# Kernel tuning notes

Hardware: AMD Instinct MI355X
Metric: run time of the kernel (lower is better)

The kernel has to match this reference:

```python
import jax, jax.numpy as jnp
import numpy as np

E, H, M, IN, T = 4, 64, 64, 32, 32      # e_size, hidden_state, message, in_size, target
HL = (128, 256, 128)                     # NNet hidden layers (priba's NNet default)
N_LAYERS = 3


def setup_inputs() -> dict:
    key = jax.random.key(0)
    ks = iter(jax.random.split(key, 64))
    B, N = 16, 128

    def w(shape, scale=0.1):
        return jax.random.normal(next(ks), shape, dtype=jnp.float32) * scale

    inp = {
        "h_in": jax.random.normal(next(ks), (B, N, IN), dtype=jnp.float32),
        "am": jax.random.normal(next(ks), (B, N, N, E), dtype=jnp.float32),
        "g_size": jax.random.randint(next(ks), (B,), 0, N),
    }
    # EdgeNetwork NNet: E -> 128 -> 256 -> 128 -> M*H
    dims_e = (E,) + HL + (M * H,)
    for i in range(4):
        inp[f"We{i}"] = w((dims_e[i], dims_e[i + 1]))
        inp[f"be{i}"] = w((dims_e[i + 1],))
    # GRU (torch nn.GRU, one layer, one step): input M, hidden H
    inp["Wih"] = w((3 * H, M)); inp["Whh"] = w((3 * H, H))
    inp["bih"] = w((3 * H,)); inp["bhh"] = w((3 * H,))
    # Readout NNets: i on [h_T, h_0] (H+IN -> T), j on h_T (H -> T)
    dims_i = (H + IN,) + HL + (T,)
    dims_j = (H,) + HL + (T,)
    for i in range(4):
        inp[f"Wi{i}"] = w((dims_i[i], dims_i[i + 1])); inp[f"bi{i}"] = w((dims_i[i + 1],))
        inp[f"Wj{i}"] = w((dims_j[i], dims_j[i + 1])); inp[f"bj{i}"] = w((dims_j[i + 1],))
    return inp


def _mlp(x, Ws, bs):
    for Wk, bk in zip(Ws[:-1], bs[:-1]):
        x = jax.nn.relu(x @ Wk + bk)
    return x @ Ws[-1] + bs[-1]


def reference(h_in, am, g_size,
              We0, be0, We1, be1, We2, be2, We3, be3,
              Wih, Whh, bih, bhh,
              Wi0, bi0, Wi1, bi1, Wi2, bi2, Wi3, bi3,
              Wj0, bj0, Wj1, bj1, Wj2, bj2, Wj3, bj3):
    B, N, _ = h_in.shape
    h = jnp.pad(h_in, ((0, 0), (0, 0), (0, H - IN)))            # pad to hidden size
    mask = (jnp.arange(N)[None, :] < g_size[:, None]).astype(h.dtype)[:, :, None]  # [B,N,1]

    # Edge-network hidden features; final linear layer is fused into the
    # message contraction to avoid materializing per-edge [M,H] matrices.
    f = am                                                       # [B,N,N,E]
    for Wk, bk in ((We0, be0), (We1, be1), (We2, be2)):
        f = jax.nn.relu(f @ Wk + bk)                             # [B,N,N,128]
    W3 = We3.reshape(HL[-1], M, H)                               # [128,M,H]
    b3 = be3.reshape(M, H)

    for _ in range(N_LAYERS):                                    # weight-tied GGNN steps
        # m[b,v,o] = sum_w (A(e_bvw) @ h_bw)[o], A = reshape(f @ We3 + be3)
        t = jnp.einsum('bvwk,bwi->bvki', f, h)                   # [B,N,128,H]
        msg = jnp.einsum('bvki,koi->bvo', t, W3)
        msg = msg + jnp.einsum('oi,bi->bo', b3, h.sum(1))[:, None, :]
        # single-step torch GRU update
        gi = msg @ Wih.T + bih
        gh = h @ Whh.T + bhh
        r = jax.nn.sigmoid(gi[..., :H] + gh[..., :H])
        z = jax.nn.sigmoid(gi[..., H:2 * H] + gh[..., H:2 * H])
        n = jnp.tanh(gi[..., 2 * H:] + r * gh[..., 2 * H:])
        h = (1.0 - z) * n + z * h
        h = h * mask

    # GGNN readout: sum_v mask * sigmoid(i([h_T, h_0])) * j(h_T), then log_softmax
    gate = jax.nn.sigmoid(_mlp(jnp.concatenate([h, h_in], -1),
                               (Wi0, Wi1, Wi2, Wi3), (bi0, bi1, bi2, bi3)))
    val = _mlp(h, (Wj0, Wj1, Wj2, Wj3), (bj0, bj1, bj2, bj3))
    res = (mask * gate * val).sum(1)                             # [B,T]
    return jax.nn.log_softmax(res, axis=1)
```

## Files before the change

kernel.cpp:

```cpp
#include <hip/hip_runtime.h>
#include <math.h>

#define B   16
#define N   128
#define E   4
#define H   64
#define M   64
#define IN_ 32
#define T   32
#define K1  128
#define K2  256
#define K3  128

typedef _Float16 f16;
typedef f16  f16x8 __attribute__((ext_vector_type(8)));
typedef float f32x4 __attribute__((ext_vector_type(4)));

#define MFMA16(a, b, c) __builtin_amdgcn_mfma_f32_16x16x32_f16(a, b, c, 0, 0, 0)

#define OFF_W1T   0
#define OFF_W2T   32768
#define OFF_WE3H  65536
#define OFF_RI0   589824
#define OFF_RI1   602112
#define OFF_RI2   634880
#define OFF_RI3   667648
#define OFF_RJ0   671744
#define OFF_RJ1   679936
#define OFF_RJ2   712704
#define OFF_RJ3   745472
#define WPACK_SZ  749568

union SmemU {
    struct { float xl[64][4]; f16 y1[64][136]; f16 y2[64][264]; } e;
    struct { f16 Al[128][72]; f16 Bl[128][72]; f16 Ol[128][136]; } pg;
    struct { float prt[4][64]; float hsum[64]; float bias[64]; } bi;
};

__global__ __launch_bounds__(256) void prep_kernel(
    const float* __restrict__ h_in,
    const float* __restrict__ We1, const float* __restrict__ We2,
    const float* __restrict__ We3,
    const float* __restrict__ Wi0, const float* __restrict__ Wi1,
    const float* __restrict__ Wi2, const float* __restrict__ Wi3,
    const float* __restrict__ Wj0, const float* __restrict__ Wj1,
    const float* __restrict__ Wj2, const float* __restrict__ Wj3,
    float* __restrict__ h, f16* __restrict__ h16, f16* __restrict__ hin16,
    f16* __restrict__ wp) {
    int idx = blockIdx.x * 256 + threadIdx.x;
    if (idx < B * N * H) {
        int i  = idx & (H - 1);
        int bn = idx >> 6;
        float v = (i < IN_) ? h_in[bn * IN_ + i] : 0.f;
        h[idx] = v;
        h16[idx] = (f16)v;
        if (i < IN_) hin16[bn * IN_ + i] = (f16)v;
    }
    if (idx >= WPACK_SZ) return;
    if (idx < OFF_W2T) {
        int j = idx >> 7, k = idx & 127;
        wp[idx] = (f16)We1[k * 256 + j];
    } else if (idx < OFF_WE3H) {
        int t = idx - OFF_W2T;
        int j = t >> 8, k = t & 255;
        wp[idx] = (f16)We2[k * 128 + j];
    } else if (idx < OFF_RI0) {
        wp[idx] = (f16)We3[idx - OFF_WE3H];
    } else if (idx < OFF_RI1) {
        int t = idx - OFF_RI0;
        int n = t / 96, c = t % 96;
        wp[idx] = (f16)Wi0[c * 128 + n];
    } else if (idx < OFF_RI2) {
        int t = idx - OFF_RI1;
        int n = t >> 7, k = t & 127;
        wp[idx] = (f16)Wi1[k * 256 + n];
    } else if (idx < OFF_RI3) {
        int t = idx - OFF_RI2;
        int n = t >> 8, k = t & 255;
        wp[idx] = (f16)Wi2[k * 128 + n];
    } else if (idx < OFF_RJ0) {
        int t = idx - OFF_RI3;
        int n = t >> 7, k = t & 127;
        wp[idx] = (f16)Wi3[k * 32 + n];
    } else if (idx < OFF_RJ1) {
        int t = idx - OFF_RJ0;
        int n = t >> 6, c = t & 63;
        wp[idx] = (f16)Wj0[c * 128 + n];
    } else if (idx < OFF_RJ2) {
        int t = idx - OFF_RJ1;
        int n = t >> 7, k = t & 127;
        wp[idx] = (f16)Wj1[k * 256 + n];
    } else if (idx < OFF_RJ3) {
        int t = idx - OFF_RJ2;
        int n = t >> 8, k = t & 255;
        wp[idx] = (f16)Wj2[k * 128 + n];
    } else {
        int t = idx - OFF_RJ3;
        int n = t >> 7, k = t & 127;
        wp[idx] = (f16)Wj3[k * 32 + n];
    }
}


__device__ void edge_body(SmemU& su, int tid, int tile,
                          const float* __restrict__ am,
                          const float* __restrict__ We0,
                          const float* __restrict__ be0,
                          const f16* __restrict__ W1t,
                          const float* __restrict__ be1,
                          const f16* __restrict__ W2t,
                          const float* __restrict__ be2,
                          f16* __restrict__ f) {
    int lane = tid & 63, wv = tid >> 6;
    long long g0 = (long long)tile * 64;

    ((float*)su.e.xl)[tid] = am[g0 * 4 + tid];
    __syncthreads();

    {
        int j = tid & 127, e0 = (tid >> 7) * 32;
        float w0 = We0[j], w1 = We0[128 + j], w2 = We0[256 + j], w3 = We0[384 + j];
        float bb = be0[j];
        #pragma unroll 8
        for (int e = e0; e < e0 + 32; ++e) {
            float v = bb + su.e.xl[e][0] * w0 + su.e.xl[e][1] * w1
                         + su.e.xl[e][2] * w2 + su.e.xl[e][3] * w3;
            su.e.y1[e][j] = (f16)fmaxf(v, 0.f);
        }
    }
    __syncthreads();

    int m = lane & 15, q = lane >> 4;

    {
        f32x4 acc[4][4];
        #pragma unroll
        for (int ct = 0; ct < 4; ++ct)
            #pragma unroll
            for (int rt = 0; rt < 4; ++rt) acc[ct][rt] = (f32x4){0.f, 0.f, 0.f, 0.f};
        #pragma unroll
        for (int s = 0; s < 4; ++s) {
            int k0 = s * 32 + q * 8;
            f16x8 afr[4], bfr[4];
            #pragma unroll
            for (int rt = 0; rt < 4; ++rt)
                afr[rt] = *(const f16x8*)&su.e.y1[rt * 16 + m][k0];
            #pragma unroll
            for (int ct = 0; ct < 4; ++ct) {
                int n = (wv * 4 + ct) * 16 + m;
                bfr[ct] = *(const f16x8*)(W1t + n * 128 + k0);
            }
            #pragma unroll
            for (int ct = 0; ct < 4; ++ct)
                #pragma unroll
                for (int rt = 0; rt < 4; ++rt)
                    acc[ct][rt] = MFMA16(afr[rt], bfr[ct], acc[ct][rt]);
        }
        #pragma unroll
        for (int ct = 0; ct < 4; ++ct) {
            int n = (wv * 4 + ct) * 16 + m;
            float bb = be1[n];
            #pragma unroll
            for (int rt = 0; rt < 4; ++rt)
                #pragma unroll
                for (int r = 0; r < 4; ++r) {
                    int row = rt * 16 + q * 4 + r;
                    su.e.y2[row][n] = (f16)fmaxf(acc[ct][rt][r] + bb, 0.f);
                }
        }
    }
    __syncthreads();

    {
        f32x4 acc[2][4];
        #pragma unroll
        for (int ct = 0; ct < 2; ++ct)
            #pragma unroll
            for (int rt = 0; rt < 4; ++rt) acc[ct][rt] = (f32x4){0.f, 0.f, 0.f, 0.f};
        #pragma unroll
        for (int s = 0; s < 8; ++s) {
            int k0 = s * 32 + q * 8;
            f16x8 afr[4], bfr[2];
            #pragma unroll
            for (int rt = 0; rt < 4; ++rt)
                afr[rt] = *(const f16x8*)&su.e.y2[rt * 16 + m][k0];
            #pragma unroll
            for (int ct = 0; ct < 2; ++ct) {
                int n = (wv * 2 + ct) * 16 + m;
                bfr[ct] = *(const f16x8*)(W2t + n * 256 + k0);
            }
            #pragma unroll
            for (int ct = 0; ct < 2; ++ct)
                #pragma unroll
                for (int rt = 0; rt < 4; ++rt)
                    acc[ct][rt] = MFMA16(afr[rt], bfr[ct], acc[ct][rt]);
        }
        #pragma unroll
        for (int ct = 0; ct < 2; ++ct) {
            int n = (wv * 2 + ct) * 16 + m;
            float bb = be2[n];
            #pragma unroll
            for (int rt = 0; rt < 4; ++rt)
                #pragma unroll
                for (int r = 0; r < 4; ++r) {
                    int row = rt * 16 + q * 4 + r;
                    su.e.y1[row][n] = (f16)fmaxf(acc[ct][rt][r] + bb, 0.f);
                }
        }
    }
    __syncthreads();

    #pragma unroll
    for (int j = 0; j < 4; ++j) {
        int c = tid + j * 256;
        int e = c >> 4, pp = c & 15;
        *(uint4*)(f + (g0 + e) * 128 + pp * 8) = *(const uint4*)&su.e.y1[e][pp * 8];
    }
}

__device__ void pgemm_body(SmemU& su, int tid, int ob, int nt,
                           const f16* __restrict__ h16,
                           const f16* __restrict__ We3h,
                           f16* __restrict__ P2) {
    int lane = tid & 63, wv = tid >> 6;

    #pragma unroll
    for (int j = 0; j < 4; ++j) {
        int c = tid + j * 256;
        int row = c >> 3, pp = c & 7;
        *(uint4*)&su.pg.Al[row][pp * 8] =
            *(const uint4*)(h16 + (size_t)(nt * 128 + row) * 64 + pp * 8);
    }
    #pragma unroll
    for (int j = 0; j < 4; ++j) {
        int c = tid + j * 256;
        int k = c >> 3, pp = c & 7;
        *(uint4*)&su.pg.Bl[k][pp * 8] =
            *(const uint4*)(We3h + ((size_t)(k * 64 + ob)) * 64 + pp * 8);
    }
    __syncthreads();

    int m = lane & 15, q = lane >> 4;
    f32x4 acc[2][8];
    #pragma unroll
    for (int ct = 0; ct < 2; ++ct)
        #pragma unroll
        for (int rt = 0; rt < 8; ++rt) acc[ct][rt] = (f32x4){0.f, 0.f, 0.f, 0.f};
    #pragma unroll
    for (int s = 0; s < 2; ++s) {
        int k0 = s * 32 + q * 8;
        f16x8 afr[8], bfr[2];
        #pragma unroll
        for (int rt = 0; rt < 8; ++rt)
            afr[rt] = *(const f16x8*)&su.pg.Al[rt * 16 + m][k0];
        #pragma unroll
        for (int ct = 0; ct < 2; ++ct)
            bfr[ct] = *(const f16x8*)&su.pg.Bl[(wv * 2 + ct) * 16 + m][k0];
        #pragma unroll
        for (int ct = 0; ct < 2; ++ct)
            #pragma unroll
            for (int rt = 0; rt < 8; ++rt)
                acc[ct][rt] = MFMA16(afr[rt], bfr[ct], acc[ct][rt]);
    }
    #pragma unroll
    for (int ct = 0; ct < 2; ++ct) {
        int col = (wv * 2 + ct) * 16 + m;
        #pragma unroll
        for (int rt = 0; rt < 8; ++rt)
            #pragma unroll
            for (int r = 0; r < 4; ++r)
                su.pg.Ol[rt * 16 + q * 4 + r][col] = (f16)acc[ct][rt][r];
    }
    __syncthreads();
    #pragma unroll
    for (int j = 0; j < 8; ++j) {
        int c = tid + j * 256;
        int row = c >> 4, pp = c & 15;
        *(uint4*)(P2 + ((size_t)(nt * 128 + row) * 64 + ob) * 128 + pp * 8) =
            *(const uint4*)&su.pg.Ol[row][pp * 8];
    }
}

__device__ void bias_body(SmemU& su, int tid, int b,
                          const float* __restrict__ h,
                          const float* __restrict__ be3,
                          float* __restrict__ biasb) {
    int i = tid & 63, wq = tid >> 6;
    float s = 0.f;
    for (int w = wq; w < N; w += 4) s += h[((size_t)(b * N + w)) * H + i];
    su.bi.prt[wq][i] = s;
    __syncthreads();
    if (tid < 64)
        su.bi.hsum[tid] = su.bi.prt[0][tid] + su.bi.prt[1][tid]
                        + su.bi.prt[2][tid] + su.bi.prt[3][tid];
    __syncthreads();
    if (tid < 64) {
        float sb = 0.f;
        #pragma unroll 4
        for (int ii = 0; ii < H; ++ii) sb += be3[tid * H + ii] * su.bi.hsum[ii];
        biasb[b * 64 + tid] = sb;
    }
}

__global__ __launch_bounds__(256, 2) void mega0_kernel(
    const float* __restrict__ am,
    const float* __restrict__ We0, const float* __restrict__ be0,
    const float* __restrict__ be1, const float* __restrict__ be2,
    const float* __restrict__ be3,
    const f16* __restrict__ wp,
    const float* __restrict__ h, const f16* __restrict__ h16,
    f16* __restrict__ f, f16* __restrict__ P2, float* __restrict__ biasb) {
    __shared__ SmemU su;
    int tid = threadIdx.x;
    int bid = blockIdx.x;
    if (bid < 4096) {
        edge_body(su, tid, bid, am, We0, be0, wp + OFF_W1T, be1, wp + OFF_W2T,
                  be2, f);
    } else if (bid < 5120) {
        int t = bid - 4096;
        pgemm_body(su, tid, t & 63, t >> 6, h16, wp + OFF_WE3H, P2);
    } else {
        bias_body(su, tid, bid - 5120, h, be3, biasb);
    }
}

__global__ __launch_bounds__(256, 2) void pg_bias_kernel(
    const float* __restrict__ be3, const f16* __restrict__ wp,
    const float* __restrict__ h, const f16* __restrict__ h16,
    f16* __restrict__ P2, float* __restrict__ biasb) {
    __shared__ SmemU su;
    int tid = threadIdx.x;
    int bid = blockIdx.x;
    if (bid < 1024) {
        pgemm_body(su, tid, bid & 63, bid >> 6, h16, wp + OFF_WE3H, P2);
    } else {
        bias_body(su, tid, bid - 1024, h, be3, biasb);
    }
}

__global__ __launch_bounds__(256, 2) void msg_mfma(
    const f16* __restrict__ f, const f16* __restrict__ P2,
    float* __restrict__ part) {
    __shared__ f16 Al[128][136];
    __shared__ f16 Bl[64][136];
    int tid = threadIdx.x, lane = tid & 63, wv = tid >> 6;
    int ws = blockIdx.x;
    int b  = blockIdx.y;
    int m = lane & 15, q = lane >> 4;

    f32x4 acc[2][4];
    #pragma unroll
    for (int rt = 0; rt < 2; ++rt)
        #pragma unroll
        for (int ct = 0; ct < 4; ++ct) acc[rt][ct] = (f32x4){0.f, 0.f, 0.f, 0.f};

    for (int wi = 0; wi < 4; ++wi) {
        int w = ws * 4 + wi;
        #pragma unroll
        for (int j = 0; j < 8; ++j) {
            int c = tid + j * 256;
            int v = c >> 4, pp = c & 15;
            *(uint4*)&Al[v][pp * 8] =
                *(const uint4*)(f + (((size_t)(b * 128 + v) * 128 + w) * 128) + pp * 8);
        }
        #pragma unroll
        for (int j = 0; j < 4; ++j) {
            int c = tid + j * 256;
            int o = c >> 4, pp = c & 15;
            *(uint4*)&Bl[o][pp * 8] =
                *(const uint4*)(P2 + (((size_t)(b * 128 + w) * 64 + o) * 128) + pp * 8);
        }
        __syncthreads();
        #pragma unroll
        for (int s = 0; s < 4; ++s) {
            int k0 = s * 32 + q * 8;
            f16x8 afr[2], bfr[4];
            #pragma unroll
            for (int rt = 0; rt < 2; ++rt)
                afr[rt] = *(const f16x8*)&Al[(wv * 2 + rt) * 16 + m][k0];
            #pragma unroll
            for (int ct = 0; ct < 4; ++ct)
                bfr[ct] = *(const f16x8*)&Bl[ct * 16 + m][k0];
            #pragma unroll
            for (int rt = 0; rt < 2; ++rt)
                #pragma unroll
                for (int ct = 0; ct < 4; ++ct)
                    acc[rt][ct] = MFMA16(afr[rt], bfr[ct], acc[rt][ct]);
        }
        __syncthreads();
    }
    float* pp = part + (size_t)ws * (2048 * 64);
    #pragma unroll
    for (int rt = 0; rt < 2; ++rt)
        #pragma unroll
        for (int ct = 0; ct < 4; ++ct) {
            int o = ct * 16 + m;
            #pragma unroll
            for (int r = 0; r < 4; ++r) {
                int v = (wv * 2 + rt) * 16 + q * 4 + r;
                pp[(size_t)(b * 128 + v) * 64 + o] = acc[rt][ct][r];
            }
        }
}

__global__ __launch_bounds__(192) void gru_kernel(
    const float* __restrict__ biasb, const float* __restrict__ part,
    float* __restrict__ h, f16* __restrict__ h16,
    const float* __restrict__ Wih, const float* __restrict__ Whh,
    const float* __restrict__ bih, const float* __restrict__ bhh,
    const int* __restrict__ g_size) {
    __shared__ float m_lds[M];
    __shared__ float h_lds[H];
    __shared__ float gi[3 * H], gh[3 * H];
    int tid = threadIdx.x;
    int bv  = blockIdx.x;
    int b = bv >> 7, v = bv & 127;

    if (tid < M) {
        float s = biasb[b * 64 + tid];
        #pragma unroll 8
        for (int sp = 0; sp < 32; ++sp)
            s += part[(size_t)sp * (2048 * 64) + bv * 64 + tid];
        m_lds[tid] = s;
    } else if (tid < M + H) {
        h_lds[tid - M] = h[bv * H + (tid - M)];
    }
    __syncthreads();

    {
        float si = bih[tid], sh = bhh[tid];
        const float* wi = Wih + tid * M;
        const float* wh = Whh + tid * H;
        #pragma unroll 4
        for (int k = 0; k < M; ++k) si += wi[k] * m_lds[k];
        #pragma unroll 4
        for (int k = 0; k < H; ++k) sh += wh[k] * h_lds[k];
        gi[tid] = si;
        gh[tid] = sh;
    }
    __syncthreads();
    if (tid < H) {
        float r = 1.f / (1.f + expf(-(gi[tid] + gh[tid])));
        float z = 1.f / (1.f + expf(-(gi[H + tid] + gh[H + tid])));
        float n = tanhf(gi[2 * H + tid] + r * gh[2 * H + tid]);
        float hv = (1.f - z) * n + z * h_lds[tid];
        float maskf = (v < g_size[b]) ? 1.f : 0.f;
        hv *= maskf;
        h[bv * H + tid] = hv;
        h16[bv * H + tid] = (f16)hv;
    }
}

__global__ __launch_bounds__(256, 4) void readout_mfma(
    const f16* __restrict__ h16, const f16* __restrict__ hin16,
    const int* __restrict__ g_size, const f16* __restrict__ wp,
    const float* __restrict__ bi0, const float* __restrict__ bi1,
    const float* __restrict__ bi2, const float* __restrict__ bi3,
    const float* __restrict__ bj0, const float* __restrict__ bj1,
    const float* __restrict__ bj2, const float* __restrict__ bj3,
    float* __restrict__ contrib) {
    __shared__ f16 Xl[32][104];
    __shared__ f16 A1[32][136];
    __shared__ f16 A2[32][264];
    __shared__ float Gl[32][36];
    const f16* Ri0 = wp + OFF_RI0; const f16* Ri1 = wp + OFF_RI1;
    const f16* Ri2 = wp + OFF_RI2; const f16* Ri3 = wp + OFF_RI3;
    const f16* Rj0 = wp + OFF_RJ0; const f16* Rj1 = wp + OFF_RJ1;
    const f16* Rj2 = wp + OFF_RJ2; const f16* Rj3 = wp + OFF_RJ3;
    int tid = threadIdx.x, lane = tid & 63, wv = tid >> 6;
    int m = lane & 15, q = lane >> 4;
    int r0 = blockIdx.x * 32;

    {
        int row = tid >> 3, pp = tid & 7;
        *(uint4*)&Xl[row][pp * 8] = *(const uint4*)(h16 + (size_t)(r0 + row) * 64 + pp * 8);
        if (tid < 128) {
            int row2 = tid >> 2, p2 = tid & 3;
            *(uint4*)&Xl[row2][64 + p2 * 8] =
                *(const uint4*)(hin16 + (size_t)(r0 + row2) * 32 + p2 * 8);
        }
    }
    __syncthreads();

    {
        f32x4 acc[2][2];
        #pragma unroll
        for (int ct = 0; ct < 2; ++ct)
            #pragma unroll
            for (int rt = 0; rt < 2; ++rt) acc[ct][rt] = (f32x4){0.f, 0.f, 0.f, 0.f};
        #pragma unroll
        for (int s = 0; s < 3; ++s) {
            int k0 = s * 32 + q * 8;
            f16x8 afr[2], bfr[2];
            #pragma unroll
            for (int rt = 0; rt < 2; ++rt) afr[rt] = *(const f16x8*)&Xl[rt * 16 + m][k0];
            #pragma unroll
            for (int ct = 0; ct < 2; ++ct)
                bfr[ct] = *(const f16x8*)(Ri0 + ((wv * 2 + ct) * 16 + m) * 96 + k0);
            #pragma unroll
            for (int ct = 0; ct < 2; ++ct)
                #pragma unroll
                for (int rt = 0; rt < 2; ++rt)
                    acc[ct][rt] = MFMA16(afr[rt], bfr[ct], acc[ct][rt]);
        }
        #pragma unroll
        for (int ct = 0; ct < 2; ++ct) {
            int n = (wv * 2 + ct) * 16 + m;
            float bb = bi0[n];
            #pragma unroll
            for (int rt = 0; rt < 2; ++rt)
                #pragma unroll
                for (int r = 0; r < 4; ++r)
                    A1[rt * 16 + q * 4 + r][n] = (f16)fmaxf(acc[ct][rt][r] + bb, 0.f);
        }
    }
    __syncthreads();

    {
        f32x4 acc[4][2];
        #pragma unroll
        for (int ct = 0; ct < 4; ++ct)
            #pragma unroll
            for (int rt = 0; rt < 2; ++rt) acc[ct][rt] = (f32x4){0.f, 0.f, 0.f, 0.f};
        #pragma unroll
        for (int s = 0; s < 4; ++s) {
            int k0 = s * 32 + q * 8;
            f16x8 afr[2], bfr[4];
            #pragma unroll
            for (int rt = 0; rt < 2; ++rt) afr[rt] = *(const f16x8*)&A1[rt * 16 + m][k0];
            #pragma unroll
            for (int ct = 0; ct < 4; ++ct)
                bfr[ct] = *(const f16x8*)(Ri1 + ((wv * 4 + ct) * 16 + m) * 128 + k0);
            #pragma unroll
            for (int ct = 0; ct < 4; ++ct)
                #pragma unroll
                for (int rt = 0; rt < 2; ++rt)
                    acc[ct][rt] = MFMA16(afr[rt], bfr[ct], acc[ct][rt]);
        }
        #pragma unroll
        for (int ct = 0; ct < 4; ++ct) {
            int n = (wv * 4 + ct) * 16 + m;
            float bb = bi1[n];
            #pragma unroll
            for (int rt = 0; rt < 2; ++rt)
                #pragma unroll
                for (int r = 0; r < 4; ++r)
                    A2[rt * 16 + q * 4 + r][n] = (f16)fmaxf(acc[ct][rt][r] + bb, 0.f);
        }
    }
    __syncthreads();

    {
        f32x4 acc[2][2];
        #pragma unroll
        for (int ct = 0; ct < 2; ++ct)
            #pragma unroll
            for (int rt = 0; rt < 2; ++rt) acc[ct][rt] = (f32x4){0.f, 0.f, 0.f, 0.f};
        #pragma unroll
        for (int s = 0; s < 8; ++s) {
            int k0 = s * 32 + q * 8;
            f16x8 afr[2], bfr[2];
            #pragma unroll
            for (int rt = 0; rt < 2; ++rt) afr[rt] = *(const f16x8*)&A2[rt * 16 + m][k0];
            #pragma unroll
            for (int ct = 0; ct < 2; ++ct)
                bfr[ct] = *(const f16x8*)(Ri2 + ((wv * 2 + ct) * 16 + m) * 256 + k0);
            #pragma unroll
            for (int ct = 0; ct < 2; ++ct)
                #pragma unroll
                for (int rt = 0; rt < 2; ++rt)
                    acc[ct][rt] = MFMA16(afr[rt], bfr[ct], acc[ct][rt]);
        }
        __syncthreads();
        #pragma unroll
        for (int ct = 0; ct < 2; ++ct) {
            int n = (wv * 2 + ct) * 16 + m;
            float bb = bi2[n];
            #pragma unroll
            for (int rt = 0; rt < 2; ++rt)
                #pragma unroll
                for (int r = 0; r < 4; ++r)
                    A1[rt * 16 + q * 4 + r][n] = (f16)fmaxf(acc[ct][rt][r] + bb, 0.f);
        }
    }
    __syncthreads();

    if (wv < 2) {
        f32x4 acc[2];
        acc[0] = (f32x4){0.f, 0.f, 0.f, 0.f};
        acc[1] = (f32x4){0.f, 0.f, 0.f, 0.f};
        int n = wv * 16 + m;
        #pragma unroll
        for (int s = 0; s < 4; ++s) {
            int k0 = s * 32 + q * 8;
            f16x8 bfr = *(const f16x8*)(Ri3 + n * 128 + k0);
            #pragma unroll
            for (int rt = 0; rt < 2; ++rt) {
                f16x8 afr = *(const f16x8*)&A1[rt * 16 + m][k0];
                acc[rt] = MFMA16(afr, bfr, acc[rt]);
            }
        }
        float bb = bi3[n];
        #pragma unroll
        for (int rt = 0; rt < 2; ++rt)
            #pragma unroll
            for (int r = 0; r < 4; ++r)
                Gl[rt * 16 + q * 4 + r][n] = 1.f / (1.f + expf(-(acc[rt][r] + bb)));
    }
    __syncthreads();

    {
        f32x4 acc[2][2];
        #pragma unroll
        for (int ct = 0; ct < 2; ++ct)
            #pragma unroll
            for (int rt = 0; rt < 2; ++rt) acc[ct][rt] = (f32x4){0.f, 0.f, 0.f, 0.f};
        #pragma unroll
        for (int s = 0; s < 2; ++s) {
            int k0 = s * 32 + q * 8;
            f16x8 afr[2], bfr[2];
            #pragma unroll
            for (int rt = 0; rt < 2; ++rt) afr[rt] = *(const f16x8*)&Xl[rt * 16 + m][k0];
            #pragma unroll
            for (int ct = 0; ct < 2; ++ct)
                bfr[ct] = *(const f16x8*)(Rj0 + ((wv * 2 + ct) * 16 + m) * 64 + k0);
            #pragma unroll
            for (int ct = 0; ct < 2; ++ct)
                #pragma unroll
                for (int rt = 0; rt < 2; ++rt)
                    acc[ct][rt] = MFMA16(afr[rt], bfr[ct], acc[ct][rt]);
        }
        __syncthreads();
        #pragma unroll
        for (int ct = 0; ct < 2; ++ct) {
            int n = (wv * 2 + ct) * 16 + m;
            float bb = bj0[n];
            #pragma unroll
            for (int rt = 0; rt < 2; ++rt)
                #pragma unroll
                for (int r = 0; r < 4; ++r)
                    A1[rt * 16 + q * 4 + r][n] = (f16)fmaxf(acc[ct][rt][r] + bb, 0.f);
        }
    }
    __syncthreads();

    {
        f32x4 acc[4][2];
        #pragma unroll
        for (int ct = 0; ct < 4; ++ct)
            #pragma unroll
            for (int rt = 0; rt < 2; ++rt) acc[ct][rt] = (f32x4){0.f, 0.f, 0.f, 0.f};
        #pragma unroll
        for (int s = 0; s < 4; ++s) {
            int k0 = s * 32 + q * 8;
            f16x8 afr[2], bfr[4];
            #pragma unroll
            for (int rt = 0; rt < 2; ++rt) afr[rt] = *(const f16x8*)&A1[rt * 16 + m][k0];
            #pragma unroll
            for (int ct = 0; ct < 4; ++ct)
                bfr[ct] = *(const f16x8*)(Rj1 + ((wv * 4 + ct) * 16 + m) * 128 + k0);
            #pragma unroll
            for (int ct = 0; ct < 4; ++ct)
                #pragma unroll
                for (int rt = 0; rt < 2; ++rt)
                    acc[ct][rt] = MFMA16(afr[rt], bfr[ct], acc[ct][rt]);
        }
        #pragma unroll
        for (int ct = 0; ct < 4; ++ct) {
            int n = (wv * 4 + ct) * 16 + m;
            float bb = bj1[n];
            #pragma unroll
            for (int rt = 0; rt < 2; ++rt)
                #pragma unroll
                for (int r = 0; r < 4; ++r)
                    A2[rt * 16 + q * 4 + r][n] = (f16)fmaxf(acc[ct][rt][r] + bb, 0.f);
        }
    }
    __syncthreads();

    {
        f32x4 acc[2][2];
        #pragma unroll
        for (int ct = 0; ct < 2; ++ct)
            #pragma unroll
            for (int rt = 0; rt < 2; ++rt) acc[ct][rt] = (f32x4){0.f, 0.f, 0.f, 0.f};
        #pragma unroll
        for (int s = 0; s < 8; ++s) {
            int k0 = s * 32 + q * 8;
            f16x8 afr[2], bfr[2];
            #pragma unroll
            for (int rt = 0; rt < 2; ++rt) afr[rt] = *(const f16x8*)&A2[rt * 16 + m][k0];
            #pragma unroll
            for (int ct = 0; ct < 2; ++ct)
                bfr[ct] = *(const f16x8*)(Rj2 + ((wv * 2 + ct) * 16 + m) * 256 + k0);
            #pragma unroll
            for (int ct = 0; ct < 2; ++ct)
                #pragma unroll
                for (int rt = 0; rt < 2; ++rt)
                    acc[ct][rt] = MFMA16(afr[rt], bfr[ct], acc[ct][rt]);
        }
        __syncthreads();
        #pragma unroll
        for (int ct = 0; ct < 2; ++ct) {
            int n = (wv * 2 + ct) * 16 + m;
            float bb = bj2[n];
            #pragma unroll
            for (int rt = 0; rt < 2; ++rt)
                #pragma unroll
                for (int r = 0; r < 4; ++r)
                    A1[rt * 16 + q * 4 + r][n] = (f16)fmaxf(acc[ct][rt][r] + bb, 0.f);
        }
    }
    __syncthreads();

    if (wv < 2) {
        f32x4 acc[2];
        acc[0] = (f32x4){0.f, 0.f, 0.f, 0.f};
        acc[1] = (f32x4){0.f, 0.f, 0.f, 0.f};
        int n = wv * 16 + m;
        #pragma unroll
        for (int s = 0; s < 4; ++s) {
            int k0 = s * 32 + q * 8;
            f16x8 bfr = *(const f16x8*)(Rj3 + n * 128 + k0);
            #pragma unroll
            for (int rt = 0; rt < 2; ++rt) {
                f16x8 afr = *(const f16x8*)&A1[rt * 16 + m][k0];
                acc[rt] = MFMA16(afr, bfr, acc[rt]);
            }
        }
        float bb = bj3[n];
        #pragma unroll
        for (int rt = 0; rt < 2; ++rt)
            #pragma unroll
            for (int r = 0; r < 4; ++r) {
                int row = rt * 16 + q * 4 + r;
                int rg = r0 + row;
                int b = rg >> 7, v = rg & 127;
                float maskf = (v < g_size[b]) ? 1.f : 0.f;
                contrib[(size_t)rg * T + n] = maskf * Gl[row][n] * (acc[rt][r] + bb);
            }
    }
}

__global__ __launch_bounds__(64) void finalize_kernel(const float* __restrict__ contrib,
                                                      float* __restrict__ out) {
    __shared__ float res[T];
    int b = blockIdx.x;
    int o = threadIdx.x;
    if (o < T) {
        float s = 0.f;
        for (int v = 0; v < N; ++v) s += contrib[(b * N + v) * T + o];
        res[o] = s;
    }
    __syncthreads();
    if (o < T) {
        float mx = res[0];
        for (int i = 1; i < T; ++i) mx = fmaxf(mx, res[i]);
        float se = 0.f;
        for (int i = 0; i < T; ++i) se += expf(res[i] - mx);
        out[b * T + o] = res[o] - mx - logf(se);
    }
}

extern "C" void kernel_launch(void* const* d_in, const int* in_sizes, int n_in,
                              void* d_out, int out_size, void* d_ws, size_t ws_size,
                              hipStream_t stream) {
    (void)in_sizes; (void)n_in; (void)out_size; (void)ws_size;
    const float* h_in = (const float*)d_in[0];
    const float* am   = (const float*)d_in[1];
    const int*   g_sz = (const int*)d_in[2];
    const float* We0 = (const float*)d_in[3],  *be0 = (const float*)d_in[4];
    const float* We1 = (const float*)d_in[5],  *be1 = (const float*)d_in[6];
    const float* We2 = (const float*)d_in[7],  *be2 = (const float*)d_in[8];
    const float* We3 = (const float*)d_in[9],  *be3 = (const float*)d_in[10];
    const float* Wih = (const float*)d_in[11], *Whh = (const float*)d_in[12];
    const float* bih = (const float*)d_in[13], *bhh = (const float*)d_in[14];
    const float* Wi0 = (const float*)d_in[15], *bi0 = (const float*)d_in[16];
    const float* Wj0 = (const float*)d_in[17], *bj0 = (const float*)d_in[18];
    const float* Wi1 = (const float*)d_in[19], *bi1 = (const float*)d_in[20];
    const float* Wj1 = (const float*)d_in[21], *bj1 = (const float*)d_in[22];
    const float* Wi2 = (const float*)d_in[23], *bi2 = (const float*)d_in[24];
    const float* Wj2 = (const float*)d_in[25], *bj2 = (const float*)d_in[26];
    const float* Wi3 = (const float*)d_in[27], *bi3 = (const float*)d_in[28];
    const float* Wj3 = (const float*)d_in[29], *bj3 = (const float*)d_in[30];

    float* out = (float*)d_out;

    f16*   f    = (f16*)d_ws;
    f16*   P2   = f + (size_t)33554432;
    float* part = (float*)(P2 + (size_t)16777216);
    float* h    = part + (size_t)4194304;
    float* biasb = h + 131072;
    float* contrib = biasb + 1024;
    f16*   h16  = (f16*)(contrib + 65536);
    f16*   hin16 = h16 + 131072;
    f16*   wp   = hin16 + 65536;

    prep_kernel<<<(WPACK_SZ + 255) / 256, 256, 0, stream>>>(
        h_in, We1, We2, We3, Wi0, Wi1, Wi2, Wi3, Wj0, Wj1, Wj2, Wj3,
        h, h16, hin16, wp);

    mega0_kernel<<<4096 + 1024 + 16, 256, 0, stream>>>(
        am, We0, be0, be1, be2, be3, wp, h, h16, f, P2, biasb);
    msg_mfma<<<dim3(32, 16), 256, 0, stream>>>(f, P2, part);
    gru_kernel<<<B * N, 192, 0, stream>>>(biasb, part, h, h16,
                                          Wih, Whh, bih, bhh, g_sz);

    for (int l = 1; l < 3; ++l) {
        pg_bias_kernel<<<1024 + 16, 256, 0, stream>>>(be3, wp, h, h16, P2, biasb);
        msg_mfma<<<dim3(32, 16), 256, 0, stream>>>(f, P2, part);
        gru_kernel<<<B * N, 192, 0, stream>>>(biasb, part, h, h16,
                                              Wih, Whh, bih, bhh, g_sz);
    }

    readout_mfma<<<64, 256, 0, stream>>>(h16, hin16, g_sz, wp,
                                         bi0, bi1, bi2, bi3,
                                         bj0, bj1, bj2, bj3, contrib);
    finalize_kernel<<<B, 64, 0, stream>>>(contrib, out);
}
```

Before: 412.1 us.

## Fuse all stages into one persistent kernel with software grid barriers

```diff
diff --git a/kernel.cpp b/kernel.cpp
--- a/kernel.cpp
+++ b/kernel.cpp
@@ -8,9 +8,6 @@
 #define M   64
 #define IN_ 32
 #define T   32
-#define K1  128
-#define K2  256
-#define K3  128
 
 typedef _Float16 f16;
 typedef f16  f16x8 __attribute__((ext_vector_type(8)));
@@ -31,96 +28,56 @@
 #define OFF_RJ3   745472
 #define WPACK_SZ  749568
 
+#define GRID_BLKS 256
+
 union SmemU {
     struct { float xl[64][4]; f16 y1[64][136]; f16 y2[64][264]; } e;
     struct { f16 Al[128][72]; f16 Bl[128][72]; f16 Ol[128][136]; } pg;
     struct { float prt[4][64]; float hsum[64]; float bias[64]; } bi;
+    struct { f16 Al[128][136]; f16 Bl[64][136]; } mm;
+    struct { f16 Xl[32][104]; f16 A1[32][136]; f16 A2[32][264]; float Gl[32][36]; } ro;
+    struct { float m_lds[64]; float h_lds[64]; float gi[192]; float gh[192]; } gr;
+    float fin[32];
 };
 
-__global__ __launch_bounds__(256) void prep_kernel(
-    const float* __restrict__ h_in,
-    const float* __restrict__ We1, const float* __restrict__ We2,
-    const float* __restrict__ We3,
-    const float* __restrict__ Wi0, const float* __restrict__ Wi1,
-    const float* __restrict__ Wi2, const float* __restrict__ Wi3,
-    const float* __restrict__ Wj0, const float* __restrict__ Wj1,
-    const float* __restrict__ Wj2, const float* __restrict__ Wj3,
-    float* __restrict__ h, f16* __restrict__ h16, f16* __restrict__ hin16,
-    f16* __restrict__ wp) {
-    int idx = blockIdx.x * 256 + threadIdx.x;
-    if (idx < B * N * H) {
-        int i  = idx & (H - 1);
-        int bn = idx >> 6;
-        float v = (i < IN_) ? h_in[bn * IN_ + i] : 0.f;
-        h[idx] = v;
-        h16[idx] = (f16)v;
-        if (i < IN_) hin16[bn * IN_ + i] = (f16)v;
-    }
-    if (idx >= WPACK_SZ) return;
-    if (idx < OFF_W2T) {
-        int j = idx >> 7, k = idx & 127;
-        wp[idx] = (f16)We1[k * 256 + j];
-    } else if (idx < OFF_WE3H) {
-        int t = idx - OFF_W2T;
-        int j = t >> 8, k = t & 255;
-        wp[idx] = (f16)We2[k * 128 + j];
-    } else if (idx < OFF_RI0) {
-        wp[idx] = (f16)We3[idx - OFF_WE3H];
-    } else if (idx < OFF_RI1) {
-        int t = idx - OFF_RI0;
-        int n = t / 96, c = t % 96;
-        wp[idx] = (f16)Wi0[c * 128 + n];
-    } else if (idx < OFF_RI2) {
-        int t = idx - OFF_RI1;
-        int n = t >> 7, k = t & 127;
-        wp[idx] = (f16)Wi1[k * 256 + n];
-    } else if (idx < OFF_RI3) {
-        int t = idx - OFF_RI2;
-        int n = t >> 8, k = t & 255;
-        wp[idx] = (f16)Wi2[k * 128 + n];
-    } else if (idx < OFF_RJ0) {
-        int t = idx - OFF_RI3;
-        int n = t >> 7, k = t & 127;
-        wp[idx] = (f16)Wi3[k * 32 + n];
-    } else if (idx < OFF_RJ1) {
-        int t = idx - OFF_RJ0;
-        int n = t >> 6, c = t & 63;
-        wp[idx] = (f16)Wj0[c * 128 + n];
-    } else if (idx < OFF_RJ2) {
-        int t = idx - OFF_RJ1;
-        int n = t >> 7, k = t & 127;
-        wp[idx] = (f16)Wj1[k * 256 + n];
-    } else if (idx < OFF_RJ3) {
-        int t = idx - OFF_RJ2;
-        int n = t >> 8, k = t & 255;
-        wp[idx] = (f16)Wj2[k * 128 + n];
-    } else {
-        int t = idx - OFF_RJ3;
-        int n = t >> 7, k = t & 127;
-        wp[idx] = (f16)Wj3[k * 32 + n];
-    }
-}
-
-
-__device__ void edge_body(SmemU& su, int tid, int tile,
-                          const float* __restrict__ am,
-                          const float* __restrict__ We0,
-                          const float* __restrict__ be0,
-                          const f16* __restrict__ W1t,
-                          const float* __restrict__ be1,
-                          const f16* __restrict__ W2t,
-                          const float* __restrict__ be2,
-                          f16* __restrict__ f) {
+struct Params {
+    const float *h_in, *am;
+    const int   *g_sz;
+    const float *We0, *be0, *We1, *be1, *We2, *be2, *We3, *be3;
+    const float *Wih, *Whh, *bih, *bhh;
+    const float *bi0, *bi1, *bi2, *bi3, *bj0, *bj1, *bj2, *bj3;
+    const float *Wi0, *Wi1, *Wi2, *Wi3, *Wj0, *Wj1, *Wj2, *Wj3;
+    f16   *f, *P2, *h16, *hin16, *wp;
+    float *msg, *h, *contrib, *out;
+    int   *bar;
+};
+
+__device__ __forceinline__ void gbar(int* bar, int ph, int tid) {
+    __syncthreads();
+    __threadfence();
+    if (tid == 0) {
+        atomicAdd(&bar[ph], 1);
+        while (atomicAdd(&bar[ph], 0) < GRID_BLKS)
+            __builtin_amdgcn_s_sleep(2);
+    }
+    __syncthreads();
+    __threadfence();
+}
+
+
+__device__ void edge_task(SmemU& su, int tid, int tile, const Params& p) {
     int lane = tid & 63, wv = tid >> 6;
     long long g0 = (long long)tile * 64;
-
-    ((float*)su.e.xl)[tid] = am[g0 * 4 + tid];
+    const f16* W1t = p.wp + OFF_W1T;
+    const f16* W2t = p.wp + OFF_W2T;
+
+    ((float*)su.e.xl)[tid] = p.am[g0 * 4 + tid];
     __syncthreads();
 
     {
         int j = tid & 127, e0 = (tid >> 7) * 32;
-        float w0 = We0[j], w1 = We0[128 + j], w2 = We0[256 + j], w3 = We0[384 + j];
-        float bb = be0[j];
+        float w0 = p.We0[j], w1 = p.We0[128 + j], w2 = p.We0[256 + j], w3 = p.We0[384 + j];
+        float bb = p.be0[j];
         #pragma unroll 8
         for (int e = e0; e < e0 + 32; ++e) {
             float v = bb + su.e.xl[e][0] * w0 + su.e.xl[e][1] * w1
@@ -159,7 +116,7 @@
         #pragma unroll
         for (int ct = 0; ct < 4; ++ct) {
             int n = (wv * 4 + ct) * 16 + m;
-            float bb = be1[n];
+            float bb = p.be1[n];
             #pragma unroll
             for (int rt = 0; rt < 4; ++rt)
                 #pragma unroll
@@ -198,7 +155,7 @@
         #pragma unroll
         for (int ct = 0; ct < 2; ++ct) {
             int n = (wv * 2 + ct) * 16 + m;
-            float bb = be2[n];
+            float bb = p.be2[n];
             #pragma unroll
             for (int rt = 0; rt < 4; ++rt)
                 #pragma unroll
@@ -214,22 +171,20 @@
     for (int j = 0; j < 4; ++j) {
         int c = tid + j * 256;
         int e = c >> 4, pp = c & 15;
-        *(uint4*)(f + (g0 + e) * 128 + pp * 8) = *(const uint4*)&su.e.y1[e][pp * 8];
-    }
-}
-
-__device__ void pgemm_body(SmemU& su, int tid, int ob, int nt,
-                           const f16* __restrict__ h16,
-                           const f16* __restrict__ We3h,
-                           f16* __restrict__ P2) {
+        *(uint4*)(p.f + (g0 + e) * 128 + pp * 8) = *(const uint4*)&su.e.y1[e][pp * 8];
+    }
+}
+
+__device__ void pgemm_task(SmemU& su, int tid, int ob, int nt, const Params& p) {
     int lane = tid & 63, wv = tid >> 6;
+    const f16* We3h = p.wp + OFF_WE3H;
 
     #pragma unroll
     for (int j = 0; j < 4; ++j) {
         int c = tid + j * 256;
         int row = c >> 3, pp = c & 7;
         *(uint4*)&su.pg.Al[row][pp * 8] =
-            *(const uint4*)(h16 + (size_t)(nt * 128 + row) * 64 + pp * 8);
+            *(const uint4*)(p.h16 + (size_t)(nt * 128 + row) * 64 + pp * 8);
     }
     #pragma unroll
     for (int j = 0; j < 4; ++j) {
@@ -276,18 +231,15 @@
     for (int j = 0; j < 8; ++j) {
         int c = tid + j * 256;
         int row = c >> 4, pp = c & 15;
-        *(uint4*)(P2 + ((size_t)(nt * 128 + row) * 64 + ob) * 128 + pp * 8) =
+        *(uint4*)(p.P2 + ((size_t)(nt * 128 + row) * 64 + ob) * 128 + pp * 8) =
             *(const uint4*)&su.pg.Ol[row][pp * 8];
     }
 }
 
-__device__ void bias_body(SmemU& su, int tid, int b,
-                          const float* __restrict__ h,
-                          const float* __restrict__ be3,
-                          float* __restrict__ biasb) {
+__device__ void bias_task(SmemU& su, int tid, int b, const Params& p) {
     int i = tid & 63, wq = tid >> 6;
     float s = 0.f;
-    for (int w = wq; w < N; w += 4) s += h[((size_t)(b * N + w)) * H + i];
+    for (int w = wq; w < N; w += 4) s += p.h[((size_t)(b * N + w)) * H + i];
     su.bi.prt[wq][i] = s;
     __syncthreads();
     if (tid < 64)
@@ -297,55 +249,16 @@
     if (tid < 64) {
         float sb = 0.f;
         #pragma unroll 4
-        for (int ii = 0; ii < H; ++ii) sb += be3[tid * H + ii] * su.bi.hsum[ii];
-        biasb[b * 64 + tid] = sb;
-    }
-}
-
-__global__ __launch_bounds__(256, 2) void mega0_kernel(
-    const float* __restrict__ am,
-    const float* __restrict__ We0, const float* __restrict__ be0,
-    const float* __restrict__ be1, const float* __restrict__ be2,
-    const float* __restrict__ be3,
-    const f16* __restrict__ wp,
-    const float* __restrict__ h, const f16* __restrict__ h16,
-    f16* __restrict__ f, f16* __restrict__ P2, float* __restrict__ biasb) {
-    __shared__ SmemU su;
-    int tid = threadIdx.x;
-    int bid = blockIdx.x;
-    if (bid < 4096) {
-        edge_body(su, tid, bid, am, We0, be0, wp + OFF_W1T, be1, wp + OFF_W2T,
-                  be2, f);
-    } else if (bid < 5120) {
-        int t = bid - 4096;
-        pgemm_body(su, tid, t & 63, t >> 6, h16, wp + OFF_WE3H, P2);
-    } else {
-        bias_body(su, tid, bid - 5120, h, be3, biasb);
-    }
-}
-
-__global__ __launch_bounds__(256, 2) void pg_bias_kernel(
-    const float* __restrict__ be3, const f16* __restrict__ wp,
-    const float* __restrict__ h, const f16* __restrict__ h16,
-    f16* __restrict__ P2, float* __restrict__ biasb) {
-    __shared__ SmemU su;
-    int tid = threadIdx.x;
-    int bid = blockIdx.x;
-    if (bid < 1024) {
-        pgemm_body(su, tid, bid & 63, bid >> 6, h16, wp + OFF_WE3H, P2);
-    } else {
-        bias_body(su, tid, bid - 1024, h, be3, biasb);
-    }
-}
-
-__global__ __launch_bounds__(256, 2) void msg_mfma(
-    const f16* __restrict__ f, const f16* __restrict__ P2,
-    float* __restrict__ part) {
-    __shared__ f16 Al[128][136];
-    __shared__ f16 Bl[64][136];
-    int tid = threadIdx.x, lane = tid & 63, wv = tid >> 6;
-    int ws = blockIdx.x;
-    int b  = blockIdx.y;
+        for (int ii = 0; ii < H; ++ii) sb += p.be3[tid * H + ii] * su.bi.hsum[ii];
+        su.bi.bias[tid] = sb;
+    }
+    __syncthreads();
+    for (int idx = tid; idx < N * M; idx += 256)
+        p.msg[(size_t)b * N * M + idx] = su.bi.bias[idx & 63];
+}
+
+__device__ void msg_task(SmemU& su, int tid, int ws, int b, const Params& p) {
+    int lane = tid & 63, wv = tid >> 6;
     int m = lane & 15, q = lane >> 4;
 
     f32x4 acc[2][4];
@@ -360,15 +273,15 @@
         for (int j = 0; j < 8; ++j) {
             int c = tid + j * 256;
             int v = c >> 4, pp = c & 15;
-            *(uint4*)&Al[v][pp * 8] =
-                *(const uint4*)(f + (((size_t)(b * 128 + v) * 128 + w) * 128) + pp * 8);
+            *(uint4*)&su.mm.Al[v][pp * 8] =
+                *(const uint4*)(p.f + (((size_t)(b * 128 + v) * 128 + w) * 128) + pp * 8);
         }
         #pragma unroll
         for (int j = 0; j < 4; ++j) {
             int c = tid + j * 256;
             int o = c >> 4, pp = c & 15;
-            *(uint4*)&Bl[o][pp * 8] =
-                *(const uint4*)(P2 + (((size_t)(b * 128 + w) * 64 + o) * 128) + pp * 8);
+            *(uint4*)&su.mm.Bl[o][pp * 8] =
+                *(const uint4*)(p.P2 + (((size_t)(b * 128 + w) * 64 + o) * 128) + pp * 8);
         }
         __syncthreads();
         #pragma unroll
@@ -377,10 +290,10 @@
             f16x8 afr[2], bfr[4];
             #pragma unroll
             for (int rt = 0; rt < 2; ++rt)
-                afr[rt] = *(const f16x8*)&Al[(wv * 2 + rt) * 16 + m][k0];
+                afr[rt] = *(const f16x8*)&su.mm.Al[(wv * 2 + rt) * 16 + m][k0];
             #pragma unroll
             for (int ct = 0; ct < 4; ++ct)
-                bfr[ct] = *(const f16x8*)&Bl[ct * 16 + m][k0];
+                bfr[ct] = *(const f16x8*)&su.mm.Bl[ct * 16 + m][k0];
             #pragma unroll
             for (int rt = 0; rt < 2; ++rt)
                 #pragma unroll
@@ -389,7 +302,6 @@
         }
         __syncthreads();
     }
-    float* pp = part + (size_t)ws * (2048 * 64);
     #pragma unroll
     for (int rt = 0; rt < 2; ++rt)
         #pragma unroll
@@ -398,86 +310,58 @@
             #pragma unroll
             for (int r = 0; r < 4; ++r) {
                 int v = (wv * 2 + rt) * 16 + q * 4 + r;
-                pp[(size_t)(b * 128 + v) * 64 + o] = acc[rt][ct][r];
+                atomicAdd(p.msg + (size_t)(b * 128 + v) * 64 + o, acc[rt][ct][r]);
             }
         }
 }
 
-__global__ __launch_bounds__(192) void gru_kernel(
-    const float* __restrict__ biasb, const float* __restrict__ part,
-    float* __restrict__ h, f16* __restrict__ h16,
-    const float* __restrict__ Wih, const float* __restrict__ Whh,
-    const float* __restrict__ bih, const float* __restrict__ bhh,
-    const int* __restrict__ g_size) {
-    __shared__ float m_lds[M];
-    __shared__ float h_lds[H];
-    __shared__ float gi[3 * H], gh[3 * H];
-    int tid = threadIdx.x;
-    int bv  = blockIdx.x;
+__device__ void gru_node(SmemU& su, int tid, int bv, const Params& p) {
     int b = bv >> 7, v = bv & 127;
-
-    if (tid < M) {
-        float s = biasb[b * 64 + tid];
-        #pragma unroll 8
-        for (int sp = 0; sp < 32; ++sp)
-            s += part[(size_t)sp * (2048 * 64) + bv * 64 + tid];
-        m_lds[tid] = s;
-    } else if (tid < M + H) {
-        h_lds[tid - M] = h[bv * H + (tid - M)];
-    }
-    __syncthreads();
-
-    {
-        float si = bih[tid], sh = bhh[tid];
-        const float* wi = Wih + tid * M;
-        const float* wh = Whh + tid * H;
+    if (tid < 64) su.gr.m_lds[tid] = p.msg[(size_t)bv * 64 + tid];
+    else if (tid < 128) su.gr.h_lds[tid - 64] = p.h[bv * 64 + (tid - 64)];
+    __syncthreads();
+    if (tid < 192) {
+        float si = p.bih[tid], sh = p.bhh[tid];
+        const float* wi = p.Wih + tid * M;
+        const float* wh = p.Whh + tid * H;
         #pragma unroll 4
-        for (int k = 0; k < M; ++k) si += wi[k] * m_lds[k];
+        for (int k = 0; k < M; ++k) si += wi[k] * su.gr.m_lds[k];
         #pragma unroll 4
-        for (int k = 0; k < H; ++k) sh += wh[k] * h_lds[k];
-        gi[tid] = si;
-        gh[tid] = sh;
-    }
-    __syncthreads();
-    if (tid < H) {
-        float r = 1.f / (1.f + expf(-(gi[tid] + gh[tid])));
-        float z = 1.f / (1.f + expf(-(gi[H + tid] + gh[H + tid])));
-        float n = tanhf(gi[2 * H + tid] + r * gh[2 * H + tid]);
-        float hv = (1.f - z) * n + z * h_lds[tid];
-        float maskf = (v < g_size[b]) ? 1.f : 0.f;
+        for (int k = 0; k < H; ++k) sh += wh[k] * su.gr.h_lds[k];
+        su.gr.gi[tid] = si;
+        su.gr.gh[tid] = sh;
+    }
+    __syncthreads();
+    if (tid < 64) {
+        float r = 1.f / (1.f + expf(-(su.gr.gi[tid] + su.gr.gh[tid])));
+        float z = 1.f / (1.f + expf(-(su.gr.gi[64 + tid] + su.gr.gh[64 + tid])));
+        float n = tanhf(su.gr.gi[128 + tid] + r * su.gr.gh[128 + tid]);
+        float hv = (1.f - z) * n + z * su.gr.h_lds[tid];
+        float maskf = (v < p.g_sz[b]) ? 1.f : 0.f;
         hv *= maskf;
-        h[bv * H + tid] = hv;
-        h16[bv * H + tid] = (f16)hv;
-    }
-}
-
-__global__ __launch_bounds__(256, 4) void readout_mfma(
-    const f16* __restrict__ h16, const f16* __restrict__ hin16,
-    const int* __restrict__ g_size, const f16* __restrict__ wp,
-    const float* __restrict__ bi0, const float* __restrict__ bi1,
-    const float* __restrict__ bi2, const float* __restrict__ bi3,
-    const float* __restrict__ bj0, const float* __restrict__ bj1,
-    const float* __restrict__ bj2, const float* __restrict__ bj3,
-    float* __restrict__ contrib) {
-    __shared__ f16 Xl[32][104];
-    __shared__ f16 A1[32][136];
-    __shared__ f16 A2[32][264];
-    __shared__ float Gl[32][36];
-    const f16* Ri0 = wp + OFF_RI0; const f16* Ri1 = wp + OFF_RI1;
-    const f16* Ri2 = wp + OFF_RI2; const f16* Ri3 = wp + OFF_RI3;
-    const f16* Rj0 = wp + OFF_RJ0; const f16* Rj1 = wp + OFF_RJ1;
-    const f16* Rj2 = wp + OFF_RJ2; const f16* Rj3 = wp + OFF_RJ3;
-    int tid = threadIdx.x, lane = tid & 63, wv = tid >> 6;
+        p.h[bv * 64 + tid] = hv;
+        p.h16[bv * 64 + tid] = (f16)hv;
+    }
+    __syncthreads();
+}
+
+__device__ void readout_task(SmemU& su, int tid, int blk, const Params& p) {
+    const f16* Ri0 = p.wp + OFF_RI0; const f16* Ri1 = p.wp + OFF_RI1;
+    const f16* Ri2 = p.wp + OFF_RI2; const f16* Ri3 = p.wp + OFF_RI3;
+    const f16* Rj0 = p.wp + OFF_RJ0; const f16* Rj1 = p.wp + OFF_RJ1;
+    const f16* Rj2 = p.wp + OFF_RJ2; const f16* Rj3 = p.wp + OFF_RJ3;
+    int lane = tid & 63, wv = tid >> 6;
     int m = lane & 15, q = lane >> 4;
-    int r0 = blockIdx.x * 32;
+    int r0 = blk * 32;
 
     {
         int row = tid >> 3, pp = tid & 7;
-        *(uint4*)&Xl[row][pp * 8] = *(const uint4*)(h16 + (size_t)(r0 + row) * 64 + pp * 8);
+        *(uint4*)&su.ro.Xl[row][pp * 8] =
+            *(const uint4*)(p.h16 + (size_t)(r0 + row) * 64 + pp * 8);
         if (tid < 128) {
             int row2 = tid >> 2, p2 = tid & 3;
-            *(uint4*)&Xl[row2][64 + p2 * 8] =
-                *(const uint4*)(hin16 + (size_t)(r0 + row2) * 32 + p2 * 8);
+            *(uint4*)&su.ro.Xl[row2][64 + p2 * 8] =
+                *(const uint4*)(p.hin16 + (size_t)(r0 + row2) * 32 + p2 * 8);
         }
     }
     __syncthreads();
@@ -493,7 +377,8 @@
             int k0 = s * 32 + q * 8;
             f16x8 afr[2], bfr[2];
             #pragma unroll
-            for (int rt = 0; rt < 2; ++rt) afr[rt] = *(const f16x8*)&Xl[rt * 16 + m][k0];
+            for (int rt = 0; rt < 2; ++rt)
+                afr[rt] = *(const f16x8*)&su.ro.Xl[rt * 16 + m][k0];
             #pragma unroll
             for (int ct = 0; ct < 2; ++ct)
                 bfr[ct] = *(const f16x8*)(Ri0 + ((wv * 2 + ct) * 16 + m) * 96 + k0);
@@ -506,12 +391,12 @@
         #pragma unroll
         for (int ct = 0; ct < 2; ++ct) {
             int n = (wv * 2 + ct) * 16 + m;
-            float bb = bi0[n];
+            float bb = p.bi0[n];
             #pragma unroll
             for (int rt = 0; rt < 2; ++rt)
                 #pragma unroll
                 for (int r = 0; r < 4; ++r)
-                    A1[rt * 16 + q * 4 + r][n] = (f16)fmaxf(acc[ct][rt][r] + bb, 0.f);
+                    su.ro.A1[rt * 16 + q * 4 + r][n] = (f16)fmaxf(acc[ct][rt][r] + bb, 0.f);
         }
     }
     __syncthreads();
@@ -527,7 +412,8 @@
             int k0 = s * 32 + q * 8;
             f16x8 afr[2], bfr[4];
             #pragma unroll
-            for (int rt = 0; rt < 2; ++rt) afr[rt] = *(const f16x8*)&A1[rt * 16 + m][k0];
+            for (int rt = 0; rt < 2; ++rt)
+                afr[rt] = *(const f16x8*)&su.ro.A1[rt * 16 + m][k0];
             #pragma unroll
             for (int ct = 0; ct < 4; ++ct)
                 bfr[ct] = *(const f16x8*)(Ri1 + ((wv * 4 + ct) * 16 + m) * 128 + k0);
@@ -540,12 +426,12 @@
         #pragma unroll
         for (int ct = 0; ct < 4; ++ct) {
             int n = (wv * 4 + ct) * 16 + m;
-            float bb = bi1[n];
+            float bb = p.bi1[n];
             #pragma unroll
             for (int rt = 0; rt < 2; ++rt)
                 #pragma unroll
                 for (int r = 0; r < 4; ++r)
-                    A2[rt * 16 + q * 4 + r][n] = (f16)fmaxf(acc[ct][rt][r] + bb, 0.f);
+                    su.ro.A2[rt * 16 + q * 4 + r][n] = (f16)fmaxf(acc[ct][rt][r] + bb, 0.f);
         }
     }
     __syncthreads();
@@ -561,7 +447,8 @@
             int k0 = s * 32 + q * 8;
             f16x8 afr[2], bfr[2];
             #pragma unroll
-            for (int rt = 0; rt < 2; ++rt) afr[rt] = *(const f16x8*)&A2[rt * 16 + m][k0];
+            for (int rt = 0; rt < 2; ++rt)
+                afr[rt] = *(const f16x8*)&su.ro.A2[rt * 16 + m][k0];
             #pragma unroll
             for (int ct = 0; ct < 2; ++ct)
                 bfr[ct] = *(const f16x8*)(Ri2 + ((wv * 2 + ct) * 16 + m) * 256 + k0);
@@ -575,12 +462,12 @@
         #pragma unroll
         for (int ct = 0; ct < 2; ++ct) {
             int n = (wv * 2 + ct) * 16 + m;
-            float bb = bi2[n];
+            float bb = p.bi2[n];
             #pragma unroll
             for (int rt = 0; rt < 2; ++rt)
                 #pragma unroll
                 for (int r = 0; r < 4; ++r)
-                    A1[rt * 16 + q * 4 + r][n] = (f16)fmaxf(acc[ct][rt][r] + bb, 0.f);
+                    su.ro.A1[rt * 16 + q * 4 + r][n] = (f16)fmaxf(acc[ct][rt][r] + bb, 0.f);
         }
     }
     __syncthreads();
@@ -596,16 +483,16 @@
             f16x8 bfr = *(const f16x8*)(Ri3 + n * 128 + k0);
             #pragma unroll
             for (int rt = 0; rt < 2; ++rt) {
-                f16x8 afr = *(const f16x8*)&A1[rt * 16 + m][k0];
+                f16x8 afr = *(const f16x8*)&su.ro.A1[rt * 16 + m][k0];
                 acc[rt] = MFMA16(afr, bfr, acc[rt]);
             }
         }
-        float bb = bi3[n];
+        float bb = p.bi3[n];
         #pragma unroll
         for (int rt = 0; rt < 2; ++rt)
             #pragma unroll
             for (int r = 0; r < 4; ++r)
-                Gl[rt * 16 + q * 4 + r][n] = 1.f / (1.f + expf(-(acc[rt][r] + bb)));
+                su.ro.Gl[rt * 16 + q * 4 + r][n] = 1.f / (1.f + expf(-(acc[rt][r] + bb)));
     }
     __syncthreads();
 
@@ -620,7 +507,8 @@
             int k0 = s * 32 + q * 8;
             f16x8 afr[2], bfr[2];
             #pragma unroll
-            for (int rt = 0; rt < 2; ++rt) afr[rt] = *(const f16x8*)&Xl[rt * 16 + m][k0];
+            for (int rt = 0; rt < 2; ++rt)
+                afr[rt] = *(const f16x8*)&su.ro.Xl[rt * 16 + m][k0];
             #pragma unroll
             for (int ct = 0; ct < 2; ++ct)
                 bfr[ct] = *(const f16x8*)(Rj0 + ((wv * 2 + ct) * 16 + m) * 64 + k0);
@@ -634,12 +522,12 @@
         #pragma unroll
         for (int ct = 0; ct < 2; ++ct) {
             int n = (wv * 2 + ct) * 16 + m;
-            float bb = bj0[n];
+            float bb = p.bj0[n];
             #pragma unroll
             for (int rt = 0; rt < 2; ++rt)
                 #pragma unroll
                 for (int r = 0; r < 4; ++r)
-                    A1[rt * 16 + q * 4 + r][n] = (f16)fmaxf(acc[ct][rt][r] + bb, 0.f);
+                    su.ro.A1[rt * 16 + q * 4 + r][n] = (f16)fmaxf(acc[ct][rt][r] + bb, 0.f);
         }
     }
     __syncthreads();
@@ -655,7 +543,8 @@
             int k0 = s * 32 + q * 8;
             f16x8 afr[2], bfr[4];
             #pragma unroll
-            for (int rt = 0; rt < 2; ++rt) afr[rt] = *(const f16x8*)&A1[rt * 16 + m][k0];
+            for (int rt = 0; rt < 2; ++rt)
+                afr[rt] = *(const f16x8*)&su.ro.A1[rt * 16 + m][k0];
             #pragma unroll
             for (int ct = 0; ct < 4; ++ct)
                 bfr[ct] = *(const f16x8*)(Rj1 + ((wv * 4 + ct) * 16 + m) * 128 + k0);
@@ -668,12 +557,12 @@
         #pragma unroll
         for (int ct = 0; ct < 4; ++ct) {
             int n = (wv * 4 + ct) * 16 + m;
-            float bb = bj1[n];
+            float bb = p.bj1[n];
             #pragma unroll
             for (int rt = 0; rt < 2; ++rt)
                 #pragma unroll
                 for (int r = 0; r < 4; ++r)
-                    A2[rt * 16 + q * 4 + r][n] = (f16)fmaxf(acc[ct][rt][r] + bb, 0.f);
+                    su.ro.A2[rt * 16 + q * 4 + r][n] = (f16)fmaxf(acc[ct][rt][r] + bb, 0.f);
         }
     }
     __syncthreads();
@@ -689,7 +578,8 @@
             int k0 = s * 32 + q * 8;
             f16x8 afr[2], bfr[2];
             #pragma unroll
-            for (int rt = 0; rt < 2; ++rt) afr[rt] = *(const f16x8*)&A2[rt * 16 + m][k0];
+            for (int rt = 0; rt < 2; ++rt)
+                afr[rt] = *(const f16x8*)&su.ro.A2[rt * 16 + m][k0];
             #pragma unroll
             for (int ct = 0; ct < 2; ++ct)
                 bfr[ct] = *(const f16x8*)(Rj2 + ((wv * 2 + ct) * 16 + m) * 256 + k0);
@@ -703,12 +593,12 @@
         #pragma unroll
         for (int ct = 0; ct < 2; ++ct) {
             int n = (wv * 2 + ct) * 16 + m;
-            float bb = bj2[n];
+            float bb = p.bj2[n];
             #pragma unroll
             for (int rt = 0; rt < 2; ++rt)
                 #pragma unroll
                 for (int r = 0; r < 4; ++r)
-                    A1[rt * 16 + q * 4 + r][n] = (f16)fmaxf(acc[ct][rt][r] + bb, 0.f);
+                    su.ro.A1[rt * 16 + q * 4 + r][n] = (f16)fmaxf(acc[ct][rt][r] + bb, 0.f);
         }
     }
     __syncthreads();
@@ -724,11 +614,11 @@
             f16x8 bfr = *(const f16x8*)(Rj3 + n * 128 + k0);
             #pragma unroll
             for (int rt = 0; rt < 2; ++rt) {
-                f16x8 afr = *(const f16x8*)&A1[rt * 16 + m][k0];
+                f16x8 afr = *(const f16x8*)&su.ro.A1[rt * 16 + m][k0];
                 acc[rt] = MFMA16(afr, bfr, acc[rt]);
             }
         }
-        float bb = bj3[n];
+        float bb = p.bj3[n];
         #pragma unroll
         for (int rt = 0; rt < 2; ++rt)
             #pragma unroll
@@ -736,85 +626,162 @@
                 int row = rt * 16 + q * 4 + r;
                 int rg = r0 + row;
                 int b = rg >> 7, v = rg & 127;
-                float maskf = (v < g_size[b]) ? 1.f : 0.f;
-                contrib[(size_t)rg * T + n] = maskf * Gl[row][n] * (acc[rt][r] + bb);
+                float maskf = (v < p.g_sz[b]) ? 1.f : 0.f;
+                p.contrib[(size_t)rg * T + n] = maskf * su.ro.Gl[row][n] * (acc[rt][r] + bb);
             }
     }
-}
-
-__global__ __launch_bounds__(64) void finalize_kernel(const float* __restrict__ contrib,
-                                                      float* __restrict__ out) {
-    __shared__ float res[T];
-    int b = blockIdx.x;
-    int o = threadIdx.x;
-    if (o < T) {
+    __syncthreads();
+}
+
+__device__ void finalize_task(SmemU& su, int tid, int b, const Params& p) {
+    if (tid < T) {
         float s = 0.f;
-        for (int v = 0; v < N; ++v) s += contrib[(b * N + v) * T + o];
-        res[o] = s;
-    }
-    __syncthreads();
-    if (o < T) {
-        float mx = res[0];
-        for (int i = 1; i < T; ++i) mx = fmaxf(mx, res[i]);
+        for (int v = 0; v < N; ++v) s += p.contrib[(b * N + v) * T + tid];
+        su.fin[tid] = s;
+    }
+    __syncthreads();
+    if (tid < T) {
+        float mx = su.fin[0];
+        for (int i = 1; i < T; ++i) mx = fmaxf(mx, su.fin[i]);
         float se = 0.f;
-        for (int i = 0; i < T; ++i) se += expf(res[i] - mx);
-        out[b * T + o] = res[o] - mx - logf(se);
-    }
+        for (int i = 0; i < T; ++i) se += expf(su.fin[i] - mx);
+        p.out[b * T + tid] = su.fin[tid] - mx - logf(se);
+    }
+    __syncthreads();
+}
+
+__global__ __launch_bounds__(256) void mega_kernel(Params p) {
+    __shared__ SmemU su;
+    int tid = threadIdx.x;
+    int bid = blockIdx.x;
+    int gidx = bid * 256 + tid;
+
+    for (int idx = gidx; idx < B * N * H; idx += GRID_BLKS * 256) {
+        int i  = idx & (H - 1);
+        int bn = idx >> 6;
+        float v = (i < IN_) ? p.h_in[bn * IN_ + i] : 0.f;
+        p.h[idx] = v;
+        p.h16[idx] = (f16)v;
+        if (i < IN_) p.hin16[bn * IN_ + i] = (f16)v;
+    }
+    for (int idx = gidx; idx < WPACK_SZ; idx += GRID_BLKS * 256) {
+        f16* wp = p.wp;
+        if (idx < OFF_W2T) {
+            int j = idx >> 7, k = idx & 127;
+            wp[idx] = (f16)p.We1[k * 256 + j];
+        } else if (idx < OFF_WE3H) {
+            int t = idx - OFF_W2T;
+            int j = t >> 8, k = t & 255;
+            wp[idx] = (f16)p.We2[k * 128 + j];
+        } else if (idx < OFF_RI0) {
+            wp[idx] = (f16)p.We3[idx - OFF_WE3H];
+        } else if (idx < OFF_RI1) {
+            int t = idx - OFF_RI0;
+            int n = t / 96, c = t % 96;
+            wp[idx] = (f16)p.Wi0[c * 128 + n];
+        } else if (idx < OFF_RI2) {
+            int t = idx - OFF_RI1;
+            int n = t >> 7, k = t & 127;
+            wp[idx] = (f16)p.Wi1[k * 256 + n];
+        } else if (idx < OFF_RI3) {
+            int t = idx - OFF_RI2;
+            int n = t >> 8, k = t & 255;
+            wp[idx] = (f16)p.Wi2[k * 128 + n];
+        } else if (idx < OFF_RJ0) {
+            int t = idx - OFF_RI3;
+            int n = t >> 7, k = t & 127;
+            wp[idx] = (f16)p.Wi3[k * 32 + n];
+        } else if (idx < OFF_RJ1) {
+            int t = idx - OFF_RJ0;
+            int n = t >> 6, c = t & 63;
+            wp[idx] = (f16)p.Wj0[c * 128 + n];
+        } else if (idx < OFF_RJ2) {
+            int t = idx - OFF_RJ1;
+            int n = t >> 7, k = t & 127;
+            wp[idx] = (f16)p.Wj1[k * 256 + n];
+        } else if (idx < OFF_RJ3) {
+            int t = idx - OFF_RJ2;
+            int n = t >> 8, k = t & 255;
+            wp[idx] = (f16)p.Wj2[k * 128 + n];
+        } else {
+            int t = idx - OFF_RJ3;
+            int n = t >> 7, k = t & 127;
+            wp[idx] = (f16)p.Wj3[k * 32 + n];
+        }
+    }
+    int ph = 0;
+    gbar(p.bar, ph++, tid);
+
+    for (int l = 0; l < 3; ++l) {
+        int ntask = (l == 0) ? (4096 + 1024 + 16) : (1024 + 16);
+        for (int t = bid; t < ntask; t += GRID_BLKS) {
+            if (l == 0) {
+                if (t < 4096)       edge_task(su, tid, t, p);
+                else if (t < 5120) { int u = t - 4096; pgemm_task(su, tid, u & 63, u >> 6, p); }
+                else                bias_task(su, tid, t - 5120, p);
+            } else {
+                if (t < 1024)       pgemm_task(su, tid, t & 63, t >> 6, p);
+                else                bias_task(su, tid, t - 1024, p);
+            }
+            __syncthreads();
+        }
+        gbar(p.bar, ph++, tid);
+
+        for (int t = bid; t < 512; t += GRID_BLKS) {
+            msg_task(su, tid, t & 31, t >> 5, p);
+            __syncthreads();
+        }
+        gbar(p.bar, ph++, tid);
+
+        for (int t = bid; t < 2048; t += GRID_BLKS)
+            gru_node(su, tid, t, p);
+        gbar(p.bar, ph++, tid);
+    }
+
+    for (int t = bid; t < 64; t += GRID_BLKS) {
+        readout_task(su, tid, t, p);
+        __syncthreads();
+    }
+    gbar(p.bar, ph++, tid);
+
+    for (int t = bid; t < 16; t += GRID_BLKS)
+        finalize_task(su, tid, t, p);
 }
 
 extern "C" void kernel_launch(void* const* d_in, const int* in_sizes, int n_in,
                               void* d_out, int out_size, void* d_ws, size_t ws_size,
                               hipStream_t stream) {
     (void)in_sizes; (void)n_in; (void)out_size; (void)ws_size;
-    const float* h_in = (const float*)d_in[0];
-    const float* am   = (const float*)d_in[1];
-    const int*   g_sz = (const int*)d_in[2];
-    const float* We0 = (const float*)d_in[3],  *be0 = (const float*)d_in[4];
-    const float* We1 = (const float*)d_in[5],  *be1 = (const float*)d_in[6];
-    const float* We2 = (const float*)d_in[7],  *be2 = (const float*)d_in[8];
-    const float* We3 = (const float*)d_in[9],  *be3 = (const float*)d_in[10];
-    const float* Wih = (const float*)d_in[11], *Whh = (const float*)d_in[12];
-    const float* bih = (const float*)d_in[13], *bhh = (const float*)d_in[14];
-    const float* Wi0 = (const float*)d_in[15], *bi0 = (const float*)d_in[16];
-    const float* Wj0 = (const float*)d_in[17], *bj0 = (const float*)d_in[18];
-    const float* Wi1 = (const float*)d_in[19], *bi1 = (const float*)d_in[20];
-    const float* Wj1 = (const float*)d_in[21], *bj1 = (const float*)d_in[22];
-    const float* Wi2 = (const float*)d_in[23], *bi2 = (const float*)d_in[24];
-    const float* Wj2 = (const float*)d_in[25], *bj2 = (const float*)d_in[26];
-    const float* Wi3 = (const float*)d_in[27], *bi3 = (const float*)d_in[28];
-    const float* Wj3 = (const float*)d_in[29], *bj3 = (const float*)d_in[30];
-
-    float* out = (float*)d_out;
-
-    f16*   f    = (f16*)d_ws;
-    f16*   P2   = f + (size_t)33554432;
-    float* part = (float*)(P2 + (size_t)16777216);
-    float* h    = part + (size_t)4194304;
-    float* biasb = h + 131072;
-    float* contrib = biasb + 1024;
-    f16*   h16  = (f16*)(contrib + 65536);
-    f16*   hin16 = h16 + 131072;
-    f16*   wp   = hin16 + 65536;
-
-    prep_kernel<<<(WPACK_SZ + 255) / 256, 256, 0, stream>>>(
-        h_in, We1, We2, We3, Wi0, Wi1, Wi2, Wi3, Wj0, Wj1, Wj2, Wj3,
-        h, h16, hin16, wp);
-
-    mega0_kernel<<<4096 + 1024 + 16, 256, 0, stream>>>(
-        am, We0, be0, be1, be2, be3, wp, h, h16, f, P2, biasb);
-    msg_mfma<<<dim3(32, 16), 256, 0, stream>>>(f, P2, part);
-    gru_kernel<<<B * N, 192, 0, stream>>>(biasb, part, h, h16,
-                                          Wih, Whh, bih, bhh, g_sz);
-
-    for (int l = 1; l < 3; ++l) {
-        pg_bias_kernel<<<1024 + 16, 256, 0, stream>>>(be3, wp, h, h16, P2, biasb);
-        msg_mfma<<<dim3(32, 16), 256, 0, stream>>>(f, P2, part);
-        gru_kernel<<<B * N, 192, 0, stream>>>(biasb, part, h, h16,
-                                              Wih, Whh, bih, bhh, g_sz);
-    }
-
-    readout_mfma<<<64, 256, 0, stream>>>(h16, hin16, g_sz, wp,
-                                         bi0, bi1, bi2, bi3,
-                                         bj0, bj1, bj2, bj3, contrib);
-    finalize_kernel<<<B, 64, 0, stream>>>(contrib, out);
-}
+    Params p;
+    p.h_in = (const float*)d_in[0];
+    p.am   = (const float*)d_in[1];
+    p.g_sz = (const int*)d_in[2];
+    p.We0 = (const float*)d_in[3];  p.be0 = (const float*)d_in[4];
+    p.We1 = (const float*)d_in[5];  p.be1 = (const float*)d_in[6];
+    p.We2 = (const float*)d_in[7];  p.be2 = (const float*)d_in[8];
+    p.We3 = (const float*)d_in[9];  p.be3 = (const float*)d_in[10];
+    p.Wih = (const float*)d_in[11]; p.Whh = (const float*)d_in[12];
+    p.bih = (const float*)d_in[13]; p.bhh = (const float*)d_in[14];
+    p.Wi0 = (const float*)d_in[15]; p.bi0 = (const float*)d_in[16];
+    p.Wj0 = (const float*)d_in[17]; p.bj0 = (const float*)d_in[18];
+    p.Wi1 = (const float*)d_in[19]; p.bi1 = (const float*)d_in[20];
+    p.Wj1 = (const float*)d_in[21]; p.bj1 = (const float*)d_in[22];
+    p.Wi2 = (const float*)d_in[23]; p.bi2 = (const float*)d_in[24];
+    p.Wj2 = (const float*)d_in[25]; p.bj2 = (const float*)d_in[26];
+    p.Wi3 = (const float*)d_in[27]; p.bi3 = (const float*)d_in[28];
+    p.Wj3 = (const float*)d_in[29]; p.bj3 = (const float*)d_in[30];
+    p.out = (float*)d_out;
+
+    p.bar   = (int*)d_ws;
+    p.f     = (f16*)((char*)d_ws + 1024);
+    p.P2    = p.f + (size_t)33554432;
+    p.msg   = (float*)(p.P2 + (size_t)16777216);
+    p.h     = p.msg + 131072;
+    p.contrib = p.h + 131072;
+    p.h16   = (f16*)(p.contrib + 65536);
+    p.hin16 = p.h16 + 131072;
+    p.wp    = p.hin16 + 65536;
+
+    hipMemsetAsync(d_ws, 0, 1024, stream);
+    mega_kernel<<<GRID_BLKS, 256, 0, stream>>>(p);
+}
```

Result: slower. 1.078 ms (+161.5%).
